# Optimization experiments

Measured on AMD Instinct MI355X. Metric: run time of the kernel, lower is better.

## Reference

```python
import jax, jax.numpy as jnp
import numpy as np

B, N, D = 32, 256, 3
NF, L = 16, 3


def _fully_connected(n):
    # Same ordering as connect_fully: for i in range(n) for j in range(n) if i != j
    a = np.repeat(np.arange(n), n)
    b = np.tile(np.arange(n), n)
    m = a != b
    return a[m].astype(np.int32), b[m].astype(np.int32)


def setup_inputs() -> dict:
    key = jax.random.key(0)
    ks = jax.random.split(key, 12)
    src, dst = _fully_connected(N)
    s = 0.1  # small param scale for numerical stability
    return {
        "xs": jax.random.normal(ks[0], (B, N, D), jnp.float32),
        "vs": jax.random.normal(ks[1], (B, N, D), jnp.float32),
        "charges": jax.random.normal(ks[2], (B * N, 1), jnp.float32),
        "W_in": s * jax.random.normal(ks[3], (1, NF), jnp.float32),
        "b_in": jnp.zeros((NF,), jnp.float32),
        "W_v": s * jax.random.normal(ks[4], (L, NF, 1), jnp.float32),
        "We1": s * jax.random.normal(ks[5], (L, 2 * NF + 1, NF), jnp.float32),
        "be1": jnp.zeros((L, NF), jnp.float32),
        "We2": s * jax.random.normal(ks[6], (L, NF, NF), jnp.float32),
        "be2": jnp.zeros((L, NF), jnp.float32),
        "Wx": s * jax.random.normal(ks[7], (L, NF, 1), jnp.float32),
        "Wh1": s * jax.random.normal(ks[8], (L, 2 * NF, NF), jnp.float32),
        "bh1": jnp.zeros((L, NF), jnp.float32),
        "src": jnp.asarray(src),
        "dst": jnp.asarray(dst),
    }


def reference(xs, vs, charges, W_in, b_in, W_v, We1, be1, We2, be2, Wx, Wh1, bh1, src, dst):
    b, n, d = xs.shape
    # node scalar features from charges (ndata['f'])
    h = jax.nn.relu(charges.reshape(b, n, 1) @ W_in + b_in)  # [B,N,nf]
    x = xs
    n_layers = We1.shape[0]
    for l in range(n_layers):
        # fully-connected edge gather + subtract (edata['d'])
        de = x[:, dst] - x[:, src]                         # [B,E,3]
        r2 = jnp.sum(de * de, axis=-1, keepdims=True)      # [B,E,1]
        e_in = jnp.concatenate([h[:, src], h[:, dst], r2], axis=-1)  # [B,E,2nf+1]
        m = jax.nn.relu(e_in @ We1[l] + be1[l])
        m = jax.nn.relu(m @ We2[l] + be2[l])               # [B,E,nf]
        w = m @ Wx[l]                                      # [B,E,1]
        # equivariant coordinate update: scatter-add edge vectors into dst nodes
        agg_x = jnp.zeros_like(x).at[:, dst].add(de * w) / (n - 1)
        x = x + agg_x + vs * (h @ W_v[l])                  # velocity term (ndata['vel'])
        m_agg = jnp.zeros_like(h).at[:, dst].add(m)        # [B,N,nf]
        h = h + jax.nn.relu(jnp.concatenate([h, m_agg], axis=-1) @ Wh1[l] + bh1[l])
    # OurDynamics returns (se3_out['1'] + xs).view(-1, n_dimension)
    return x.reshape(-1, d)
```

## Files before the change

kernel.cpp:

```cpp
#include <hip/hip_runtime.h>

#define BB 32
#define NN 256
#define NF 16

typedef _Float16 half4 __attribute__((ext_vector_type(4)));
typedef float f32x4 __attribute__((ext_vector_type(4)));

#define X0_OFF 0
#define X1_OFF 32768
#define H0_OFF 65536
#define H1_OFF 196608

__device__ __forceinline__ float dot4(float4 a, float4 b, float acc) {
    acc = fmaf(a.x, b.x, acc); acc = fmaf(a.y, b.y, acc);
    acc = fmaf(a.z, b.z, acc); acc = fmaf(a.w, b.w, acc);
    return acc;
}

__global__ __launch_bounds__(256)
void layer_kernel(const float* __restrict__ xs, const float* __restrict__ charges,
                  const float* __restrict__ W_in, const float* __restrict__ b_in,
                  const float* __restrict__ x_in, const float* __restrict__ h_in,
                  float* __restrict__ x_out, float* __restrict__ h_out,
                  const float* __restrict__ vs, const float* __restrict__ Wv_l,
                  const float* __restrict__ We1_l, const float* __restrict__ be1_l,
                  const float* __restrict__ We2_l, const float* __restrict__ be2_l,
                  const float* __restrict__ Wx_l, const float* __restrict__ Wh1_l,
                  const float* __restrict__ bh1_l,
                  int first_layer, int final_layer) {
    __shared__ __align__(16) float  su[NN * 20];
    __shared__ __align__(16) float4 sx[NN];
    __shared__ __align__(16) float  sWaT[256];
    __shared__ __align__(16) float  sWbT[256];
    __shared__ float  sWh1s[512];
    __shared__ __align__(16) float  sh8[8][NF];
    __shared__ float  svd[8][NF];
    __shared__ float  sg[8][NF];
    __shared__ float  sWin[NF], sbin[NF], sbe1[NF];

    const int tid  = threadIdx.x;
    const int b    = blockIdx.x >> 5;
    const int oct  = blockIdx.x & 31;
    const int n0l  = 8 * oct;
    const size_t n0 = (size_t)b * NN + n0l;
    const int w    = tid >> 6;
    const int lane = tid & 63;
    const int c    = lane & 15;
    const int g    = lane >> 4;

    {
        const int f = tid >> 4, k = tid & 15;
        sWaT[k * NF + f] = We1_l[tid];
        sWbT[k * NF + f] = We1_l[256 + tid];
    }
    sWh1s[tid]       = Wh1_l[tid];
    sWh1s[256 + tid] = Wh1_l[256 + tid];
    if (tid < NF) {
        sbe1[tid] = be1_l[tid];
        if (first_layer) { sWin[tid] = W_in[tid]; sbin[tid] = b_in[tid]; }
    }
    if (first_layer) {
        const size_t n = (size_t)b * NN + tid;
        sx[tid] = make_float4(xs[n * 3 + 0], xs[n * 3 + 1], xs[n * 3 + 2], 0.f);
        if (tid < 128) {
            const int jd = tid >> 4, f = tid & 15;
            sh8[jd][f] = fmaxf(fmaf(charges[n0 + jd], W_in[f], b_in[f]), 0.f);
        }
    } else {
        sx[tid] = ((const float4*)x_in)[(size_t)b * NN + tid];
        if (tid < 32) {
            const int jd = tid >> 2, q = tid & 3;
            *(float4*)&sh8[jd][4 * q] =
                ((const float4*)(h_in + (n0 + jd) * NF))[q];
        }
    }
    __syncthreads();

    {
        float4 hq0, hq1, hq2, hq3;
        if (first_layer) {
            const float cc = charges[(size_t)b * NN + tid];
            hq0 = make_float4(fmaxf(fmaf(cc, sWin[0], sbin[0]), 0.f),
                              fmaxf(fmaf(cc, sWin[1], sbin[1]), 0.f),
                              fmaxf(fmaf(cc, sWin[2], sbin[2]), 0.f),
                              fmaxf(fmaf(cc, sWin[3], sbin[3]), 0.f));
            hq1 = make_float4(fmaxf(fmaf(cc, sWin[4], sbin[4]), 0.f),
                              fmaxf(fmaf(cc, sWin[5], sbin[5]), 0.f),
                              fmaxf(fmaf(cc, sWin[6], sbin[6]), 0.f),
                              fmaxf(fmaf(cc, sWin[7], sbin[7]), 0.f));
            hq2 = make_float4(fmaxf(fmaf(cc, sWin[8], sbin[8]), 0.f),
                              fmaxf(fmaf(cc, sWin[9], sbin[9]), 0.f),
                              fmaxf(fmaf(cc, sWin[10], sbin[10]), 0.f),
                              fmaxf(fmaf(cc, sWin[11], sbin[11]), 0.f));
            hq3 = make_float4(fmaxf(fmaf(cc, sWin[12], sbin[12]), 0.f),
                              fmaxf(fmaf(cc, sWin[13], sbin[13]), 0.f),
                              fmaxf(fmaf(cc, sWin[14], sbin[14]), 0.f),
                              fmaxf(fmaf(cc, sWin[15], sbin[15]), 0.f));
        } else {
            const float4* h4 = (const float4*)(h_in + ((size_t)b * NN + tid) * NF);
            hq0 = h4[0]; hq1 = h4[1]; hq2 = h4[2]; hq3 = h4[3];
        }
#pragma unroll
        for (int q = 0; q < 4; ++q) {
            float4 uq;
            {
                const float4* wt = (const float4*)&sWaT[(4 * q + 0) * NF];
                uq.x = dot4(hq3, wt[3], dot4(hq2, wt[2], dot4(hq1, wt[1], dot4(hq0, wt[0], 0.f))));
            }
            {
                const float4* wt = (const float4*)&sWaT[(4 * q + 1) * NF];
                uq.y = dot4(hq3, wt[3], dot4(hq2, wt[2], dot4(hq1, wt[1], dot4(hq0, wt[0], 0.f))));
            }
            {
                const float4* wt = (const float4*)&sWaT[(4 * q + 2) * NF];
                uq.z = dot4(hq3, wt[3], dot4(hq2, wt[2], dot4(hq1, wt[1], dot4(hq0, wt[0], 0.f))));
            }
            {
                const float4* wt = (const float4*)&sWaT[(4 * q + 3) * NF];
                uq.w = dot4(hq3, wt[3], dot4(hq2, wt[2], dot4(hq1, wt[1], dot4(hq0, wt[0], 0.f))));
            }
            *(float4*)&su[tid * 20 + 4 * q] = uq;
        }
    }
    if (tid < 128) {
        const int jd = tid >> 4, k = tid & 15;
        const float4* hj = (const float4*)&sh8[jd][0];
        const float4* wt = (const float4*)&sWbT[k * NF];
        float v = sbe1[k];
        v = dot4(hj[0], wt[0], v);
        v = dot4(hj[1], wt[1], v);
        v = dot4(hj[2], wt[2], v);
        v = dot4(hj[3], wt[3], v);
        svd[jd][k] = v;
    }
    half4 afrag;
    afrag.x = (_Float16)We2_l[(4 * g + 0) * NF + c];
    afrag.y = (_Float16)We2_l[(4 * g + 1) * NF + c];
    afrag.z = (_Float16)We2_l[(4 * g + 2) * NF + c];
    afrag.w = (_Float16)We2_l[(4 * g + 3) * NF + c];
    const float4 wr4  = *(const float4*)(We1_l + 512 + 4 * g);
    const float4 be2f = *(const float4*)(be2_l + 4 * g);
    const float4 wxf  = *(const float4*)(Wx_l + 4 * g);
    __syncthreads();

    const int j0 = n0l + w, j1 = n0l + 4 + w;
    const float4 xj0 = sx[j0];
    const float4 xj1 = sx[j1];
    const float4 v40 = *(const float4*)&svd[w][4 * g];
    const float4 v41 = *(const float4*)&svd[w + 4][4 * g];

    float Sw0 = 0.f, Swx0 = 0.f, Swy0 = 0.f, Swz0 = 0.f;
    float Sw1 = 0.f, Swx1 = 0.f, Swy1 = 0.f, Swz1 = 0.f;
    float g00 = 0.f, g01 = 0.f, g02 = 0.f, g03 = 0.f;
    float g10 = 0.f, g11 = 0.f, g12 = 0.f, g13 = 0.f;

#pragma unroll 2
    for (int t = 0; t < 16; ++t) {
        const int s = 16 * t + c;
        const float4 u4  = *(const float4*)&su[s * 20 + 4 * g];
        const float4 xs4 = sx[s];
        const f32x4 zc = {0.f, 0.f, 0.f, 0.f};
        {
            const float dx = xj0.x - xs4.x, dy = xj0.y - xs4.y, dz = xj0.z - xs4.z;
            const float r2 = fmaf(dx, dx, fmaf(dy, dy, dz * dz));
            const float m0 = fmaxf(fmaf(r2, wr4.x, u4.x + v40.x), 0.f);
            const float m1 = fmaxf(fmaf(r2, wr4.y, u4.y + v40.y), 0.f);
            const float m2 = fmaxf(fmaf(r2, wr4.z, u4.z + v40.z), 0.f);
            const float m3 = fmaxf(fmaf(r2, wr4.w, u4.w + v40.w), 0.f);
            half4 bfrag;
            bfrag.x = (_Float16)m0; bfrag.y = (_Float16)m1;
            bfrag.z = (_Float16)m2; bfrag.w = (_Float16)m3;
            const f32x4 acc = __builtin_amdgcn_mfma_f32_16x16x16f16(afrag, bfrag, zc, 0, 0, 0);
            const float e0 = fmaxf(acc.x + be2f.x, 0.f);
            const float e1 = fmaxf(acc.y + be2f.y, 0.f);
            const float e2 = fmaxf(acc.z + be2f.z, 0.f);
            const float e3 = fmaxf(acc.w + be2f.w, 0.f);
            float wp = e0 * wxf.x;
            wp = fmaf(e1, wxf.y, wp);
            wp = fmaf(e2, wxf.z, wp);
            wp = fmaf(e3, wxf.w, wp);
            const float gsel = (s != j0) ? 1.f : 0.f;
            g00 = fmaf(e0, gsel, g00);
            g01 = fmaf(e1, gsel, g01);
            g02 = fmaf(e2, gsel, g02);
            g03 = fmaf(e3, gsel, g03);
            Sw0 += wp;
            Swx0 = fmaf(wp, xs4.x, Swx0);
            Swy0 = fmaf(wp, xs4.y, Swy0);
            Swz0 = fmaf(wp, xs4.z, Swz0);
        }
        {
            const float dx = xj1.x - xs4.x, dy = xj1.y - xs4.y, dz = xj1.z - xs4.z;
            const float r2 = fmaf(dx, dx, fmaf(dy, dy, dz * dz));
            const float m0 = fmaxf(fmaf(r2, wr4.x, u4.x + v41.x), 0.f);
            const float m1 = fmaxf(fmaf(r2, wr4.y, u4.y + v41.y), 0.f);
            const float m2 = fmaxf(fmaf(r2, wr4.z, u4.z + v41.z), 0.f);
            const float m3 = fmaxf(fmaf(r2, wr4.w, u4.w + v41.w), 0.f);
            half4 bfrag;
            bfrag.x = (_Float16)m0; bfrag.y = (_Float16)m1;
            bfrag.z = (_Float16)m2; bfrag.w = (_Float16)m3;
            const f32x4 acc = __builtin_amdgcn_mfma_f32_16x16x16f16(afrag, bfrag, zc, 0, 0, 0);
            const float e0 = fmaxf(acc.x + be2f.x, 0.f);
            const float e1 = fmaxf(acc.y + be2f.y, 0.f);
            const float e2 = fmaxf(acc.z + be2f.z, 0.f);
            const float e3 = fmaxf(acc.w + be2f.w, 0.f);
            float wp = e0 * wxf.x;
            wp = fmaf(e1, wxf.y, wp);
            wp = fmaf(e2, wxf.z, wp);
            wp = fmaf(e3, wxf.w, wp);
            const float gsel = (s != j1) ? 1.f : 0.f;
            g10 = fmaf(e0, gsel, g10);
            g11 = fmaf(e1, gsel, g11);
            g12 = fmaf(e2, gsel, g12);
            g13 = fmaf(e3, gsel, g13);
            Sw1 += wp;
            Swx1 = fmaf(wp, xs4.x, Swx1);
            Swy1 = fmaf(wp, xs4.y, Swy1);
            Swz1 = fmaf(wp, xs4.z, Swz1);
        }
    }

#pragma unroll
    for (int off = 1; off < 64; off <<= 1) {
        Sw0  += __shfl_xor(Sw0,  off, 64);  Sw1  += __shfl_xor(Sw1,  off, 64);
        Swx0 += __shfl_xor(Swx0, off, 64);  Swx1 += __shfl_xor(Swx1, off, 64);
        Swy0 += __shfl_xor(Swy0, off, 64);  Swy1 += __shfl_xor(Swy1, off, 64);
        Swz0 += __shfl_xor(Swz0, off, 64);  Swz1 += __shfl_xor(Swz1, off, 64);
    }
#pragma unroll
    for (int off = 1; off < 16; off <<= 1) {
        g00 += __shfl_xor(g00, off, 64);  g10 += __shfl_xor(g10, off, 64);
        g01 += __shfl_xor(g01, off, 64);  g11 += __shfl_xor(g11, off, 64);
        g02 += __shfl_xor(g02, off, 64);  g12 += __shfl_xor(g12, off, 64);
        g03 += __shfl_xor(g03, off, 64);  g13 += __shfl_xor(g13, off, 64);
    }
    if ((lane & 15) == 0) {
        *(float4*)&sg[w][4 * g]     = make_float4(g00, g01, g02, g03);
        *(float4*)&sg[w + 4][4 * g] = make_float4(g10, g11, g12, g13);
    }
    __syncthreads();

    const int is0 = (lane < 16);
    const int is1 = (lane >= 32 && lane < 48);
    if (is0 || is1) {
        const int f = lane & 15;
        const int slot = is0 ? w : (w + 4);
        const int jm   = is0 ? j0 : j1;
        const float SwS = is0 ? Sw0  : Sw1;
        const float SxS = is0 ? Swx0 : Swx1;
        const float SyS = is0 ? Swy0 : Swy1;
        const float SzS = is0 ? Swz0 : Swz1;
        const float4 xjm = is0 ? xj0 : xj1;
        const size_t nj = (size_t)b * NN + jm;
        float hd = bh1_l[f];
        float hv = 0.f;
#pragma unroll
        for (int k = 0; k < NF; ++k) {
            const float hjk = sh8[slot][k];
            hd = fmaf(hjk, sWh1s[k * NF + f], hd);
            hv = fmaf(hjk, Wv_l[k], hv);
        }
#pragma unroll
        for (int k = 0; k < NF; ++k) {
            hd = fmaf(sg[slot][k], sWh1s[(NF + k) * NF + f], hd);
        }
        const float hnew = sh8[slot][f] + fmaxf(hd, 0.f);
        if (!final_layer) h_out[nj * NF + f] = hnew;
        if (f < 3) {
            const float xc = (f == 0) ? xjm.x : ((f == 1) ? xjm.y : xjm.z);
            const float Sc = (f == 0) ? SxS  : ((f == 1) ? SyS  : SzS);
            const float agg = (SwS * xc - Sc) * (1.f / 255.f);
            const float xnew = xc + agg + vs[nj * 3 + f] * hv;
            if (final_layer) x_out[nj * 3 + f] = xnew;
            else             x_out[nj * 4 + f] = xnew;
        }
        if (!final_layer && f == 3) x_out[nj * 4 + 3] = 0.f;
    }
}

extern "C" void kernel_launch(void* const* d_in, const int* in_sizes, int n_in,
                              void* d_out, int out_size, void* d_ws, size_t ws_size,
                              hipStream_t stream) {
    const float* xs      = (const float*)d_in[0];
    const float* vs      = (const float*)d_in[1];
    const float* charges = (const float*)d_in[2];
    const float* W_in    = (const float*)d_in[3];
    const float* b_in    = (const float*)d_in[4];
    const float* W_v     = (const float*)d_in[5];
    const float* We1     = (const float*)d_in[6];
    const float* be1     = (const float*)d_in[7];
    const float* We2     = (const float*)d_in[8];
    const float* be2     = (const float*)d_in[9];
    const float* Wx      = (const float*)d_in[10];
    const float* Wh1     = (const float*)d_in[11];
    const float* bh1     = (const float*)d_in[12];

    float* ws = (float*)d_ws;
    float* x0 = ws + X0_OFF;
    float* x1 = ws + X1_OFF;
    float* h0 = ws + H0_OFF;
    float* h1 = ws + H1_OFF;
    float* out = (float*)d_out;

    hipLaunchKernelGGL(layer_kernel, dim3(1024), dim3(256), 0, stream,
                       xs, charges, W_in, b_in, x0, h0, x1, h1,
                       vs, W_v + 0 * 16, We1 + 0 * 528, be1 + 0 * 16, We2 + 0 * 256,
                       be2 + 0 * 16, Wx + 0 * 16, Wh1 + 0 * 512, bh1 + 0 * 16, 1, 0);
    hipLaunchKernelGGL(layer_kernel, dim3(1024), dim3(256), 0, stream,
                       xs, charges, W_in, b_in, x1, h1, x0, h0,
                       vs, W_v + 1 * 16, We1 + 1 * 528, be1 + 1 * 16, We2 + 1 * 256,
                       be2 + 1 * 16, Wx + 1 * 16, Wh1 + 1 * 512, bh1 + 1 * 16, 0, 0);
    hipLaunchKernelGGL(layer_kernel, dim3(1024), dim3(256), 0, stream,
                       xs, charges, W_in, b_in, x0, h0, out, h1,
                       vs, W_v + 2 * 16, We1 + 2 * 528, be1 + 2 * 16, We2 + 2 * 256,
                       be2 + 2 * 16, Wx + 2 * 16, Wh1 + 2 * 512, bh1 + 2 * 16, 0, 1);
}
```

Before: 143.0 us.

## Fuse all three layers into one persistent kernel with grid barriers

Replaces three per-layer launches with one persistent kernel of 1024 blocks that syncs between layers through a global atomic barrier. Node features h stay in shared memory across layers. The per-node projection u = h·We1a is now computed once per node and written to global workspace, instead of every block recomputing it for all 256 nodes of its batch. The edge loop now reads x and u from global memory (L2) rather than LDS. Correctness depends on all 1024 blocks being co-resident. The barrier counters and the MAGIC flag are reset racily between calls, which risks hangs or stale barrier state on repeated invocations.

```diff
diff --git a/kernel.cpp b/kernel.cpp
--- a/kernel.cpp
+++ b/kernel.cpp
@@ -3,14 +3,12 @@
 #define BB 32
 #define NN 256
 #define NF 16
+#define NBLK 1024
+#define MAGIC 0x1357913
 
 typedef _Float16 half4 __attribute__((ext_vector_type(4)));
 typedef float f32x4 __attribute__((ext_vector_type(4)));
 
-#define X0_OFF 0
-#define X1_OFF 32768
-#define H0_OFF 65536
-#define H1_OFF 196608
 
 __device__ __forceinline__ float dot4(float4 a, float4 b, float acc) {
     acc = fmaf(a.x, b.x, acc); acc = fmaf(a.y, b.y, acc);
@@ -18,26 +16,39 @@
     return acc;
 }
 
-__global__ __launch_bounds__(256)
-void layer_kernel(const float* __restrict__ xs, const float* __restrict__ charges,
-                  const float* __restrict__ W_in, const float* __restrict__ b_in,
-                  const float* __restrict__ x_in, const float* __restrict__ h_in,
-                  float* __restrict__ x_out, float* __restrict__ h_out,
-                  const float* __restrict__ vs, const float* __restrict__ Wv_l,
-                  const float* __restrict__ We1_l, const float* __restrict__ be1_l,
-                  const float* __restrict__ We2_l, const float* __restrict__ be2_l,
-                  const float* __restrict__ Wx_l, const float* __restrict__ Wh1_l,
-                  const float* __restrict__ bh1_l,
-                  int first_layer, int final_layer) {
-    __shared__ __align__(16) float  su[NN * 20];
-    __shared__ __align__(16) float4 sx[NN];
-    __shared__ __align__(16) float  sWaT[256];
-    __shared__ __align__(16) float  sWbT[256];
-    __shared__ float  sWh1s[512];
-    __shared__ __align__(16) float  sh8[8][NF];
-    __shared__ float  svd[8][NF];
-    __shared__ float  sg[8][NF];
-    __shared__ float  sWin[NF], sbin[NF], sbe1[NF];
+__device__ __forceinline__ void gbar(int* bar, int which) {
+    __syncthreads();
+    if (threadIdx.x == 0) {
+        __threadfence();
+        const int old = atomicAdd(&bar[1 + which], 1);
+        if (old == NBLK - 1) {
+            __hip_atomic_store(&bar[4 + which], 1, __ATOMIC_RELEASE,
+                               __HIP_MEMORY_SCOPE_AGENT);
+        } else {
+            while (__hip_atomic_load(&bar[4 + which], __ATOMIC_ACQUIRE,
+                                     __HIP_MEMORY_SCOPE_AGENT) == 0)
+                __builtin_amdgcn_s_sleep(1);
+        }
+    }
+    __syncthreads();
+}
+
+__global__ __launch_bounds__(256, 4)
+void fused_kernel(const float* __restrict__ xs, const float* __restrict__ vs,
+                  const float* __restrict__ charges, const float* __restrict__ W_in,
+                  const float* __restrict__ b_in, const float* __restrict__ W_v,
+                  const float* __restrict__ We1, const float* __restrict__ be1,
+                  const float* __restrict__ We2, const float* __restrict__ be2,
+                  const float* __restrict__ Wx, const float* __restrict__ Wh1,
+                  const float* __restrict__ bh1, float* __restrict__ out,
+                  float* __restrict__ ws) {
+    __shared__ __align__(16) float sWaT[256];
+    __shared__ __align__(16) float sWbT[256];
+    __shared__ float sWh1s[512];
+    __shared__ __align__(16) float sh8[8][NF];
+    __shared__ float svd[8][NF];
+    __shared__ float sg[8][NF];
+    __shared__ float sbe1[NF];
 
     const int tid  = threadIdx.x;
     const int b    = blockIdx.x >> 5;
@@ -49,233 +60,252 @@
     const int c    = lane & 15;
     const int g    = lane >> 4;
 
+    float* x0  = ws;
+    float* x1  = ws + 32768;
+    float* su0 = ws + 65536;
+    float* su1 = ws + 196608;
+    int*   bar = (int*)(ws + 327680);
+
+    if (blockIdx.x == 0 && tid == 0) {
+        bar[1] = 0; bar[2] = 0; bar[3] = 0;
+        bar[4] = 0; bar[5] = 0; bar[6] = 0;
+        __hip_atomic_store(&bar[0], MAGIC, __ATOMIC_RELEASE, __HIP_MEMORY_SCOPE_AGENT);
+    }
+    if (tid == 0) {
+        while (__hip_atomic_load(&bar[0], __ATOMIC_ACQUIRE,
+                                 __HIP_MEMORY_SCOPE_AGENT) != MAGIC)
+            __builtin_amdgcn_s_sleep(1);
+    }
+    __syncthreads();
+
     {
         const int f = tid >> 4, k = tid & 15;
-        sWaT[k * NF + f] = We1_l[tid];
-        sWbT[k * NF + f] = We1_l[256 + tid];
-    }
-    sWh1s[tid]       = Wh1_l[tid];
-    sWh1s[256 + tid] = Wh1_l[256 + tid];
-    if (tid < NF) {
-        sbe1[tid] = be1_l[tid];
-        if (first_layer) { sWin[tid] = W_in[tid]; sbin[tid] = b_in[tid]; }
-    }
-    if (first_layer) {
-        const size_t n = (size_t)b * NN + tid;
-        sx[tid] = make_float4(xs[n * 3 + 0], xs[n * 3 + 1], xs[n * 3 + 2], 0.f);
-        if (tid < 128) {
-            const int jd = tid >> 4, f = tid & 15;
-            sh8[jd][f] = fmaxf(fmaf(charges[n0 + jd], W_in[f], b_in[f]), 0.f);
-        }
-    } else {
-        sx[tid] = ((const float4*)x_in)[(size_t)b * NN + tid];
-        if (tid < 32) {
-            const int jd = tid >> 2, q = tid & 3;
-            *(float4*)&sh8[jd][4 * q] =
-                ((const float4*)(h_in + (n0 + jd) * NF))[q];
-        }
+        sWaT[k * NF + f] = We1[tid];
+    }
+    if (tid < 128) {
+        const int jd = tid >> 4, f = tid & 15;
+        sh8[jd][f] = fmaxf(fmaf(charges[n0 + jd], W_in[f], b_in[f]), 0.f);
+    }
+    if (tid < 32) {
+        const int jd = tid >> 2, q = tid & 3;
+        x0[(n0 + jd) * 4 + q] = (q < 3) ? xs[(n0 + jd) * 3 + q] : 0.f;
     }
     __syncthreads();
-
-    {
-        float4 hq0, hq1, hq2, hq3;
-        if (first_layer) {
-            const float cc = charges[(size_t)b * NN + tid];
-            hq0 = make_float4(fmaxf(fmaf(cc, sWin[0], sbin[0]), 0.f),
-                              fmaxf(fmaf(cc, sWin[1], sbin[1]), 0.f),
-                              fmaxf(fmaf(cc, sWin[2], sbin[2]), 0.f),
-                              fmaxf(fmaf(cc, sWin[3], sbin[3]), 0.f));
-            hq1 = make_float4(fmaxf(fmaf(cc, sWin[4], sbin[4]), 0.f),
-                              fmaxf(fmaf(cc, sWin[5], sbin[5]), 0.f),
-                              fmaxf(fmaf(cc, sWin[6], sbin[6]), 0.f),
-                              fmaxf(fmaf(cc, sWin[7], sbin[7]), 0.f));
-            hq2 = make_float4(fmaxf(fmaf(cc, sWin[8], sbin[8]), 0.f),
-                              fmaxf(fmaf(cc, sWin[9], sbin[9]), 0.f),
-                              fmaxf(fmaf(cc, sWin[10], sbin[10]), 0.f),
-                              fmaxf(fmaf(cc, sWin[11], sbin[11]), 0.f));
-            hq3 = make_float4(fmaxf(fmaf(cc, sWin[12], sbin[12]), 0.f),
-                              fmaxf(fmaf(cc, sWin[13], sbin[13]), 0.f),
-                              fmaxf(fmaf(cc, sWin[14], sbin[14]), 0.f),
-                              fmaxf(fmaf(cc, sWin[15], sbin[15]), 0.f));
-        } else {
-            const float4* h4 = (const float4*)(h_in + ((size_t)b * NN + tid) * NF);
-            hq0 = h4[0]; hq1 = h4[1]; hq2 = h4[2]; hq3 = h4[3];
-        }
-#pragma unroll
-        for (int q = 0; q < 4; ++q) {
-            float4 uq;
-            {
-                const float4* wt = (const float4*)&sWaT[(4 * q + 0) * NF];
-                uq.x = dot4(hq3, wt[3], dot4(hq2, wt[2], dot4(hq1, wt[1], dot4(hq0, wt[0], 0.f))));
-            }
-            {
-                const float4* wt = (const float4*)&sWaT[(4 * q + 1) * NF];
-                uq.y = dot4(hq3, wt[3], dot4(hq2, wt[2], dot4(hq1, wt[1], dot4(hq0, wt[0], 0.f))));
-            }
-            {
-                const float4* wt = (const float4*)&sWaT[(4 * q + 2) * NF];
-                uq.z = dot4(hq3, wt[3], dot4(hq2, wt[2], dot4(hq1, wt[1], dot4(hq0, wt[0], 0.f))));
-            }
-            {
-                const float4* wt = (const float4*)&sWaT[(4 * q + 3) * NF];
-                uq.w = dot4(hq3, wt[3], dot4(hq2, wt[2], dot4(hq1, wt[1], dot4(hq0, wt[0], 0.f))));
-            }
-            *(float4*)&su[tid * 20 + 4 * q] = uq;
-        }
-    }
     if (tid < 128) {
         const int jd = tid >> 4, k = tid & 15;
         const float4* hj = (const float4*)&sh8[jd][0];
-        const float4* wt = (const float4*)&sWbT[k * NF];
-        float v = sbe1[k];
-        v = dot4(hj[0], wt[0], v);
-        v = dot4(hj[1], wt[1], v);
-        v = dot4(hj[2], wt[2], v);
-        v = dot4(hj[3], wt[3], v);
-        svd[jd][k] = v;
-    }
-    half4 afrag;
-    afrag.x = (_Float16)We2_l[(4 * g + 0) * NF + c];
-    afrag.y = (_Float16)We2_l[(4 * g + 1) * NF + c];
-    afrag.z = (_Float16)We2_l[(4 * g + 2) * NF + c];
-    afrag.w = (_Float16)We2_l[(4 * g + 3) * NF + c];
-    const float4 wr4  = *(const float4*)(We1_l + 512 + 4 * g);
-    const float4 be2f = *(const float4*)(be2_l + 4 * g);
-    const float4 wxf  = *(const float4*)(Wx_l + 4 * g);
-    __syncthreads();
-
-    const int j0 = n0l + w, j1 = n0l + 4 + w;
-    const float4 xj0 = sx[j0];
-    const float4 xj1 = sx[j1];
-    const float4 v40 = *(const float4*)&svd[w][4 * g];
-    const float4 v41 = *(const float4*)&svd[w + 4][4 * g];
-
-    float Sw0 = 0.f, Swx0 = 0.f, Swy0 = 0.f, Swz0 = 0.f;
-    float Sw1 = 0.f, Swx1 = 0.f, Swy1 = 0.f, Swz1 = 0.f;
-    float g00 = 0.f, g01 = 0.f, g02 = 0.f, g03 = 0.f;
-    float g10 = 0.f, g11 = 0.f, g12 = 0.f, g13 = 0.f;
+        const float4* wt = (const float4*)&sWaT[k * NF];
+        float u = dot4(hj[0], wt[0], 0.f);
+        u = dot4(hj[1], wt[1], u);
+        u = dot4(hj[2], wt[2], u);
+        u = dot4(hj[3], wt[3], u);
+        su0[(n0 + jd) * NF + k] = u;
+    }
+    gbar(bar, 0);
+
+#pragma unroll 1
+    for (int l = 0; l < 3; ++l) {
+        const int final_layer = (l == 2);
+        const float* We1_l = We1 + l * 528;
+        const float* We2_l = We2 + l * 256;
+        const float* Wv_l  = W_v + l * NF;
+        const float* be2_l = be2 + l * NF;
+        const float* Wx_l  = Wx  + l * NF;
+        const float* Wh1_l = Wh1 + l * 512;
+        const float* bh1_l = bh1 + l * NF;
+        const float* x_cur  = (l == 1) ? x1 : x0;
+        float*       x_nxt  = (l == 0) ? x1 : x0;
+        const float* su_cur = (l == 1) ? su1 : su0;
+        float*       su_nxt = (l == 0) ? su1 : su0;
+
+        __syncthreads();
+        {
+            const int f = tid >> 4, k = tid & 15;
+            sWbT[k * NF + f] = We1_l[256 + tid];
+            if (!final_layer) sWaT[k * NF + f] = We1[(l + 1) * 528 + tid];
+        }
+        sWh1s[tid]       = Wh1_l[tid];
+        sWh1s[256 + tid] = Wh1_l[256 + tid];
+        if (tid < NF) sbe1[tid] = be1[l * NF + tid];
+        half4 afrag;
+        afrag.x = (_Float16)We2_l[(4 * g + 0) * NF + c];
+        afrag.y = (_Float16)We2_l[(4 * g + 1) * NF + c];
+        afrag.z = (_Float16)We2_l[(4 * g + 2) * NF + c];
+        afrag.w = (_Float16)We2_l[(4 * g + 3) * NF + c];
+        const float4 wr4  = *(const float4*)(We1_l + 512 + 4 * g);
+        const float4 be2f = *(const float4*)(be2_l + 4 * g);
+        const float4 wxf  = *(const float4*)(Wx_l + 4 * g);
+        __syncthreads();
+
+        if (tid < 128) {
+            const int jd = tid >> 4, k = tid & 15;
+            const float4* hj = (const float4*)&sh8[jd][0];
+            const float4* wt = (const float4*)&sWbT[k * NF];
+            float v = sbe1[k];
+            v = dot4(hj[0], wt[0], v);
+            v = dot4(hj[1], wt[1], v);
+            v = dot4(hj[2], wt[2], v);
+            v = dot4(hj[3], wt[3], v);
+            svd[jd][k] = v;
+        }
+        __syncthreads();
+
+        const int j0 = n0l + w, j1 = n0l + 4 + w;
+        const float* x_b  = x_cur + (size_t)b * NN * 4;
+        const float* su_b = su_cur + (size_t)b * NN * NF;
+        const float4 xj0 = *(const float4*)(x_b + 4 * j0);
+        const float4 xj1 = *(const float4*)(x_b + 4 * j1);
+        const float4 v40 = *(const float4*)&svd[w][4 * g];
+        const float4 v41 = *(const float4*)&svd[w + 4][4 * g];
+
+        float Sw0 = 0.f, Swx0 = 0.f, Swy0 = 0.f, Swz0 = 0.f;
+        float Sw1 = 0.f, Swx1 = 0.f, Swy1 = 0.f, Swz1 = 0.f;
+        float g00 = 0.f, g01 = 0.f, g02 = 0.f, g03 = 0.f;
+        float g10 = 0.f, g11 = 0.f, g12 = 0.f, g13 = 0.f;
+
+        const float* su_p = su_b + c * NF + 4 * g;
+        const float* x_p  = x_b + 4 * c;
 
 #pragma unroll 2
-    for (int t = 0; t < 16; ++t) {
-        const int s = 16 * t + c;
-        const float4 u4  = *(const float4*)&su[s * 20 + 4 * g];
-        const float4 xs4 = sx[s];
-        const f32x4 zc = {0.f, 0.f, 0.f, 0.f};
-        {
-            const float dx = xj0.x - xs4.x, dy = xj0.y - xs4.y, dz = xj0.z - xs4.z;
-            const float r2 = fmaf(dx, dx, fmaf(dy, dy, dz * dz));
-            const float m0 = fmaxf(fmaf(r2, wr4.x, u4.x + v40.x), 0.f);
-            const float m1 = fmaxf(fmaf(r2, wr4.y, u4.y + v40.y), 0.f);
-            const float m2 = fmaxf(fmaf(r2, wr4.z, u4.z + v40.z), 0.f);
-            const float m3 = fmaxf(fmaf(r2, wr4.w, u4.w + v40.w), 0.f);
-            half4 bfrag;
-            bfrag.x = (_Float16)m0; bfrag.y = (_Float16)m1;
-            bfrag.z = (_Float16)m2; bfrag.w = (_Float16)m3;
-            const f32x4 acc = __builtin_amdgcn_mfma_f32_16x16x16f16(afrag, bfrag, zc, 0, 0, 0);
-            const float e0 = fmaxf(acc.x + be2f.x, 0.f);
-            const float e1 = fmaxf(acc.y + be2f.y, 0.f);
-            const float e2 = fmaxf(acc.z + be2f.z, 0.f);
-            const float e3 = fmaxf(acc.w + be2f.w, 0.f);
-            float wp = e0 * wxf.x;
-            wp = fmaf(e1, wxf.y, wp);
-            wp = fmaf(e2, wxf.z, wp);
-            wp = fmaf(e3, wxf.w, wp);
-            const float gsel = (s != j0) ? 1.f : 0.f;
-            g00 = fmaf(e0, gsel, g00);
-            g01 = fmaf(e1, gsel, g01);
-            g02 = fmaf(e2, gsel, g02);
-            g03 = fmaf(e3, gsel, g03);
-            Sw0 += wp;
-            Swx0 = fmaf(wp, xs4.x, Swx0);
-            Swy0 = fmaf(wp, xs4.y, Swy0);
-            Swz0 = fmaf(wp, xs4.z, Swz0);
-        }
-        {
-            const float dx = xj1.x - xs4.x, dy = xj1.y - xs4.y, dz = xj1.z - xs4.z;
-            const float r2 = fmaf(dx, dx, fmaf(dy, dy, dz * dz));
-            const float m0 = fmaxf(fmaf(r2, wr4.x, u4.x + v41.x), 0.f);
-            const float m1 = fmaxf(fmaf(r2, wr4.y, u4.y + v41.y), 0.f);
-            const float m2 = fmaxf(fmaf(r2, wr4.z, u4.z + v41.z), 0.f);
-            const float m3 = fmaxf(fmaf(r2, wr4.w, u4.w + v41.w), 0.f);
-            half4 bfrag;
-            bfrag.x = (_Float16)m0; bfrag.y = (_Float16)m1;
-            bfrag.z = (_Float16)m2; bfrag.w = (_Float16)m3;
-            const f32x4 acc = __builtin_amdgcn_mfma_f32_16x16x16f16(afrag, bfrag, zc, 0, 0, 0);
-            const float e0 = fmaxf(acc.x + be2f.x, 0.f);
-            const float e1 = fmaxf(acc.y + be2f.y, 0.f);
-            const float e2 = fmaxf(acc.z + be2f.z, 0.f);
-            const float e3 = fmaxf(acc.w + be2f.w, 0.f);
-            float wp = e0 * wxf.x;
-            wp = fmaf(e1, wxf.y, wp);
-            wp = fmaf(e2, wxf.z, wp);
-            wp = fmaf(e3, wxf.w, wp);
-            const float gsel = (s != j1) ? 1.f : 0.f;
-            g10 = fmaf(e0, gsel, g10);
-            g11 = fmaf(e1, gsel, g11);
-            g12 = fmaf(e2, gsel, g12);
-            g13 = fmaf(e3, gsel, g13);
-            Sw1 += wp;
-            Swx1 = fmaf(wp, xs4.x, Swx1);
-            Swy1 = fmaf(wp, xs4.y, Swy1);
-            Swz1 = fmaf(wp, xs4.z, Swz1);
-        }
-    }
+        for (int t = 0; t < 16; ++t) {
+            const float4 u4  = *(const float4*)(su_p + 256 * t);
+            const float4 xs4 = *(const float4*)(x_p + 64 * t);
+            const f32x4 zc = {0.f, 0.f, 0.f, 0.f};
+            const int s = 16 * t + c;
+            {
+                const float dx = xj0.x - xs4.x, dy = xj0.y - xs4.y, dz = xj0.z - xs4.z;
+                const float r2 = fmaf(dx, dx, fmaf(dy, dy, dz * dz));
+                const float m0 = fmaxf(fmaf(r2, wr4.x, u4.x + v40.x), 0.f);
+                const float m1 = fmaxf(fmaf(r2, wr4.y, u4.y + v40.y), 0.f);
+                const float m2 = fmaxf(fmaf(r2, wr4.z, u4.z + v40.z), 0.f);
+                const float m3 = fmaxf(fmaf(r2, wr4.w, u4.w + v40.w), 0.f);
+                half4 bfrag;
+                bfrag.x = (_Float16)m0; bfrag.y = (_Float16)m1;
+                bfrag.z = (_Float16)m2; bfrag.w = (_Float16)m3;
+                const f32x4 acc = __builtin_amdgcn_mfma_f32_16x16x16f16(afrag, bfrag, zc, 0, 0, 0);
+                const float e0 = fmaxf(acc.x + be2f.x, 0.f);
+                const float e1 = fmaxf(acc.y + be2f.y, 0.f);
+                const float e2 = fmaxf(acc.z + be2f.z, 0.f);
+                const float e3 = fmaxf(acc.w + be2f.w, 0.f);
+                float wp = e0 * wxf.x;
+                wp = fmaf(e1, wxf.y, wp);
+                wp = fmaf(e2, wxf.z, wp);
+                wp = fmaf(e3, wxf.w, wp);
+                const float gsel = (s != j0) ? 1.f : 0.f;
+                g00 = fmaf(e0, gsel, g00);
+                g01 = fmaf(e1, gsel, g01);
+                g02 = fmaf(e2, gsel, g02);
+                g03 = fmaf(e3, gsel, g03);
+                Sw0 += wp;
+                Swx0 = fmaf(wp, xs4.x, Swx0);
+                Swy0 = fmaf(wp, xs4.y, Swy0);
+                Swz0 = fmaf(wp, xs4.z, Swz0);
+            }
+            {
+                const float dx = xj1.x - xs4.x, dy = xj1.y - xs4.y, dz = xj1.z - xs4.z;
+                const float r2 = fmaf(dx, dx, fmaf(dy, dy, dz * dz));
+                const float m0 = fmaxf(fmaf(r2, wr4.x, u4.x + v41.x), 0.f);
+                const float m1 = fmaxf(fmaf(r2, wr4.y, u4.y + v41.y), 0.f);
+                const float m2 = fmaxf(fmaf(r2, wr4.z, u4.z + v41.z), 0.f);
+                const float m3 = fmaxf(fmaf(r2, wr4.w, u4.w + v41.w), 0.f);
+                half4 bfrag;
+                bfrag.x = (_Float16)m0; bfrag.y = (_Float16)m1;
+                bfrag.z = (_Float16)m2; bfrag.w = (_Float16)m3;
+                const f32x4 acc = __builtin_amdgcn_mfma_f32_16x16x16f16(afrag, bfrag, zc, 0, 0, 0);
+                const float e0 = fmaxf(acc.x + be2f.x, 0.f);
+                const float e1 = fmaxf(acc.y + be2f.y, 0.f);
+                const float e2 = fmaxf(acc.z + be2f.z, 0.f);
+                const float e3 = fmaxf(acc.w + be2f.w, 0.f);
+                float wp = e0 * wxf.x;
+                wp = fmaf(e1, wxf.y, wp);
+                wp = fmaf(e2, wxf.z, wp);
+                wp = fmaf(e3, wxf.w, wp);
+                const float gsel = (s != j1) ? 1.f : 0.f;
+                g10 = fmaf(e0, gsel, g10);
+                g11 = fmaf(e1, gsel, g11);
+                g12 = fmaf(e2, gsel, g12);
+                g13 = fmaf(e3, gsel, g13);
+                Sw1 += wp;
+                Swx1 = fmaf(wp, xs4.x, Swx1);
+                Swy1 = fmaf(wp, xs4.y, Swy1);
+                Swz1 = fmaf(wp, xs4.z, Swz1);
+            }
+        }
 
 #pragma unroll
-    for (int off = 1; off < 64; off <<= 1) {
-        Sw0  += __shfl_xor(Sw0,  off, 64);  Sw1  += __shfl_xor(Sw1,  off, 64);
-        Swx0 += __shfl_xor(Swx0, off, 64);  Swx1 += __shfl_xor(Swx1, off, 64);
-        Swy0 += __shfl_xor(Swy0, off, 64);  Swy1 += __shfl_xor(Swy1, off, 64);
-        Swz0 += __shfl_xor(Swz0, off, 64);  Swz1 += __shfl_xor(Swz1, off, 64);
-    }
+        for (int off = 1; off < 64; off <<= 1) {
+            Sw0  += __shfl_xor(Sw0,  off, 64);  Sw1  += __shfl_xor(Sw1,  off, 64);
+            Swx0 += __shfl_xor(Swx0, off, 64);  Swx1 += __shfl_xor(Swx1, off, 64);
+            Swy0 += __shfl_xor(Swy0, off, 64);  Swy1 += __shfl_xor(Swy1, off, 64);
+            Swz0 += __shfl_xor(Swz0, off, 64);  Swz1 += __shfl_xor(Swz1, off, 64);
+        }
 #pragma unroll
-    for (int off = 1; off < 16; off <<= 1) {
-        g00 += __shfl_xor(g00, off, 64);  g10 += __shfl_xor(g10, off, 64);
-        g01 += __shfl_xor(g01, off, 64);  g11 += __shfl_xor(g11, off, 64);
-        g02 += __shfl_xor(g02, off, 64);  g12 += __shfl_xor(g12, off, 64);
-        g03 += __shfl_xor(g03, off, 64);  g13 += __shfl_xor(g13, off, 64);
-    }
-    if ((lane & 15) == 0) {
-        *(float4*)&sg[w][4 * g]     = make_float4(g00, g01, g02, g03);
-        *(float4*)&sg[w + 4][4 * g] = make_float4(g10, g11, g12, g13);
-    }
-    __syncthreads();
-
-    const int is0 = (lane < 16);
-    const int is1 = (lane >= 32 && lane < 48);
-    if (is0 || is1) {
-        const int f = lane & 15;
-        const int slot = is0 ? w : (w + 4);
-        const int jm   = is0 ? j0 : j1;
-        const float SwS = is0 ? Sw0  : Sw1;
-        const float SxS = is0 ? Swx0 : Swx1;
-        const float SyS = is0 ? Swy0 : Swy1;
-        const float SzS = is0 ? Swz0 : Swz1;
-        const float4 xjm = is0 ? xj0 : xj1;
-        const size_t nj = (size_t)b * NN + jm;
-        float hd = bh1_l[f];
-        float hv = 0.f;
+        for (int off = 1; off < 16; off <<= 1) {
+            g00 += __shfl_xor(g00, off, 64);  g10 += __shfl_xor(g10, off, 64);
+            g01 += __shfl_xor(g01, off, 64);  g11 += __shfl_xor(g11, off, 64);
+            g02 += __shfl_xor(g02, off, 64);  g12 += __shfl_xor(g12, off, 64);
+            g03 += __shfl_xor(g03, off, 64);  g13 += __shfl_xor(g13, off, 64);
+        }
+        if ((lane & 15) == 0) {
+            *(float4*)&sg[w][4 * g]     = make_float4(g00, g01, g02, g03);
+            *(float4*)&sg[w + 4][4 * g] = make_float4(g10, g11, g12, g13);
+        }
+        __syncthreads();
+
+        const int is0 = (lane < 16);
+        const int is1 = (lane >= 32 && lane < 48);
+        float hnew = 0.f;
+        int slot = 0;
+        if (is0 || is1) {
+            const int f = lane & 15;
+            slot = is0 ? w : (w + 4);
+            const int jm   = is0 ? j0 : j1;
+            const float SwS = is0 ? Sw0  : Sw1;
+            const float SxS = is0 ? Swx0 : Swx1;
+            const float SyS = is0 ? Swy0 : Swy1;
+            const float SzS = is0 ? Swz0 : Swz1;
+            const float4 xjm = is0 ? xj0 : xj1;
+            const size_t nj = (size_t)b * NN + jm;
+            float hd = bh1_l[f];
+            float hv = 0.f;
 #pragma unroll
-        for (int k = 0; k < NF; ++k) {
-            const float hjk = sh8[slot][k];
-            hd = fmaf(hjk, sWh1s[k * NF + f], hd);
-            hv = fmaf(hjk, Wv_l[k], hv);
-        }
+            for (int k = 0; k < NF; ++k) {
+                const float hjk = sh8[slot][k];
+                hd = fmaf(hjk, sWh1s[k * NF + f], hd);
+                hv = fmaf(hjk, Wv_l[k], hv);
+            }
 #pragma unroll
-        for (int k = 0; k < NF; ++k) {
-            hd = fmaf(sg[slot][k], sWh1s[(NF + k) * NF + f], hd);
-        }
-        const float hnew = sh8[slot][f] + fmaxf(hd, 0.f);
-        if (!final_layer) h_out[nj * NF + f] = hnew;
-        if (f < 3) {
-            const float xc = (f == 0) ? xjm.x : ((f == 1) ? xjm.y : xjm.z);
-            const float Sc = (f == 0) ? SxS  : ((f == 1) ? SyS  : SzS);
-            const float agg = (SwS * xc - Sc) * (1.f / 255.f);
-            const float xnew = xc + agg + vs[nj * 3 + f] * hv;
-            if (final_layer) x_out[nj * 3 + f] = xnew;
-            else             x_out[nj * 4 + f] = xnew;
-        }
-        if (!final_layer && f == 3) x_out[nj * 4 + 3] = 0.f;
+            for (int k = 0; k < NF; ++k) {
+                hd = fmaf(sg[slot][k], sWh1s[(NF + k) * NF + f], hd);
+            }
+            hnew = sh8[slot][f] + fmaxf(hd, 0.f);
+            if (f < 3) {
+                const float xc = (f == 0) ? xjm.x : ((f == 1) ? xjm.y : xjm.z);
+                const float Sc = (f == 0) ? SxS  : ((f == 1) ? SyS  : SzS);
+                const float agg = (SwS * xc - Sc) * (1.f / 255.f);
+                const float xnew = xc + agg + vs[nj * 3 + f] * hv;
+                if (final_layer) out[nj * 3 + f] = xnew;
+                else             x_nxt[nj * 4 + f] = xnew;
+            }
+            if (!final_layer && f == 3) x_nxt[nj * 4 + 3] = 0.f;
+        }
+        __syncthreads();
+        if (is0 || is1) sh8[slot][lane & 15] = hnew;
+
+        if (!final_layer) {
+            __syncthreads();
+            if (tid < 128) {
+                const int jd = tid >> 4, k = tid & 15;
+                const float4* hj = (const float4*)&sh8[jd][0];
+                const float4* wt = (const float4*)&sWaT[k * NF];
+                float u = dot4(hj[0], wt[0], 0.f);
+                u = dot4(hj[1], wt[1], u);
+                u = dot4(hj[2], wt[2], u);
+                u = dot4(hj[3], wt[3], u);
+                su_nxt[(n0 + jd) * NF + k] = u;
+            }
+            gbar(bar, l + 1);
+        }
     }
 }
 
@@ -296,23 +326,10 @@
     const float* Wh1     = (const float*)d_in[11];
     const float* bh1     = (const float*)d_in[12];
 
-    float* ws = (float*)d_ws;
-    float* x0 = ws + X0_OFF;
-    float* x1 = ws + X1_OFF;
-    float* h0 = ws + H0_OFF;
-    float* h1 = ws + H1_OFF;
+    float* ws  = (float*)d_ws;
     float* out = (float*)d_out;
 
-    hipLaunchKernelGGL(layer_kernel, dim3(1024), dim3(256), 0, stream,
-                       xs, charges, W_in, b_in, x0, h0, x1, h1,
-                       vs, W_v + 0 * 16, We1 + 0 * 528, be1 + 0 * 16, We2 + 0 * 256,
-                       be2 + 0 * 16, Wx + 0 * 16, Wh1 + 0 * 512, bh1 + 0 * 16, 1, 0);
-    hipLaunchKernelGGL(layer_kernel, dim3(1024), dim3(256), 0, stream,
-                       xs, charges, W_in, b_in, x1, h1, x0, h0,
-                       vs, W_v + 1 * 16, We1 + 1 * 528, be1 + 1 * 16, We2 + 1 * 256,
-                       be2 + 1 * 16, Wx + 1 * 16, Wh1 + 1 * 512, bh1 + 1 * 16, 0, 0);
-    hipLaunchKernelGGL(layer_kernel, dim3(1024), dim3(256), 0, stream,
-                       xs, charges, W_in, b_in, x0, h0, out, h1,
-                       vs, W_v + 2 * 16, We1 + 2 * 528, be1 + 2 * 16, We2 + 2 * 256,
-                       be2 + 2 * 16, Wx + 2 * 16, Wh1 + 2 * 512, bh1 + 2 * 16, 0, 1);
+    hipLaunchKernelGGL(fused_kernel, dim3(NBLK), dim3(256), 0, stream,
+                       xs, vs, charges, W_in, b_in, W_v, We1, be1, We2, be2,
+                       Wx, Wh1, bh1, out, ws);
 }
```

Result: slower. 516.1 us (+261.0%).
